# Kernel optimization log

Hardware: AMD Instinct MI355X
Metric: run time of the kernel (lower is better)

Reference implementation:

```python
import jax, jax.numpy as jnp
import numpy as np

B, S, K, N = 4, 2048, 4096, 4096


def setup_inputs() -> dict:
    key = jax.random.key(0)
    kx, kw = jax.random.split(key)
    # int8 activations and weights in [-127, 127), matching torch.randint(-127,127,...)
    x = jax.random.randint(kx, (B, S, K), -127, 127, dtype=jnp.int32).astype(jnp.int8)
    weight = jax.random.randint(kw, (N, K), -127, 127, dtype=jnp.int32).astype(jnp.int8)
    bias = jnp.zeros((1, N), dtype=jnp.int32)
    out_scale = jnp.ones((), dtype=jnp.float32)
    bias_scale = jnp.ones((), dtype=jnp.float32)
    return {"x": x, "weight": weight, "bias": bias,
            "out_scale": out_scale, "bias_scale": bias_scale}


def reference(x, weight, bias, out_scale, bias_scale):
    # Flatten leading dims: [B, S, K] -> [M, K]
    x_shape = x.shape
    x2 = x.reshape(-1, x_shape[-1])
    acc = jax.lax.dot_general(
        x2, weight,
        dimension_numbers=(((1,), (1,)), ((), ())),
        preferred_element_type=jnp.int32,
    )  # [M, N] int32
    # Fused epilogue: y = round(out_scale * acc + bias_scale * bias) -> int32
    y = jnp.round(acc.astype(jnp.float32) * out_scale
                  + bias.astype(jnp.float32) * bias_scale).astype(jnp.int32)
    return y.reshape(*x_shape[:-1], -1)
```

## Files before the change

kernel.cpp:

```cpp
#include <hip/hip_runtime.h>
#include <stdint.h>


typedef int v4i __attribute__((ext_vector_type(4)));

#define BM 128
#define BN 128
#define BK 64
#define KK 4096

__global__ __launch_bounds__(256)
void pack_i32_to_i8(const v4i* __restrict__ src, int* __restrict__ dst, int n4) {
    int i = blockIdx.x * blockDim.x + threadIdx.x;
    if (i >= n4) return;
    v4i a = src[i];
    dst[i] = (a[0] & 0xff) | ((a[1] & 0xff) << 8) | ((a[2] & 0xff) << 16) | (a[3] << 24);
}

__device__ __forceinline__ void gld_lds16(const void* g, void* lds) {
    __builtin_amdgcn_global_load_lds(
        (const __attribute__((address_space(1))) unsigned int*)g,
        (__attribute__((address_space(3))) unsigned int*)lds,
        16, 0, 0);
}

__global__ __launch_bounds__(256, 2)
void w8a8_gemm_kernel(const int8_t* __restrict__ X,
                      const int8_t* __restrict__ W,
                      const int*    __restrict__ bias,
                      const float*  __restrict__ out_scale_p,
                      const float*  __restrict__ bias_scale_p,
                      int*          __restrict__ Y,
                      int M, int N)
{
    __shared__ __align__(16) int8_t sA[BM * BK];
    __shared__ __align__(16) int8_t sB[BN * BK];

    const int t = threadIdx.x;
    const int w = t >> 6;
    const int l = t & 63;
    const int wm = w >> 1;
    const int wn = w & 1;

    const int bn = blockIdx.x * BN;
    const int bm = blockIdx.y * BM;

    const float out_scale  = *out_scale_p;
    const float bias_scale = *bias_scale_p;

    const int8_t* Abase = X + (size_t)bm * KK;
    const int8_t* Bbase = W + (size_t)bn * KK;

    const int c0 = w * 64 + l;
    const int c1 = 256 + c0;
    const int ga0 = (c0 >> 2) * KK + (c0 & 3) * 16;
    const int ga1 = (c1 >> 2) * KK + (c1 & 3) * 16;

    int8_t* sA_r0 = sA + w * 1024;
    int8_t* sA_r1 = sA + 4096 + w * 1024;
    int8_t* sB_r0 = sB + w * 1024;
    int8_t* sB_r1 = sB + 4096 + w * 1024;

    const int tm   = l & 15;
    const int quad = l >> 4;
    const int ldsA = (wm * 64 + tm) * BK + quad * 16;
    const int ldsB = (wn * 64 + tm) * BK + quad * 16;

    v4i acc[4][4];
    const v4i vzero = {0, 0, 0, 0};
#pragma unroll
    for (int i = 0; i < 4; i++)
#pragma unroll
        for (int j = 0; j < 4; j++)
            acc[i][j] = vzero;

    for (int k0 = 0; k0 < KK; k0 += BK) {
        gld_lds16(Abase + ga0 + k0, sA_r0);
        gld_lds16(Abase + ga1 + k0, sA_r1);
        gld_lds16(Bbase + ga0 + k0, sB_r0);
        gld_lds16(Bbase + ga1 + k0, sB_r1);
        __syncthreads();

        v4i a[4], b[4];
#pragma unroll
        for (int i = 0; i < 4; i++)
            a[i] = *(const v4i*)(sA + ldsA + i * 16 * BK);
#pragma unroll
        for (int j = 0; j < 4; j++)
            b[j] = *(const v4i*)(sB + ldsB + j * 16 * BK);

#pragma unroll
        for (int i = 0; i < 4; i++)
#pragma unroll
            for (int j = 0; j < 4; j++)
                acc[i][j] = __builtin_amdgcn_mfma_i32_16x16x64_i8(a[i], b[j], acc[i][j], 0, 0, 0);

        __syncthreads();
    }

#pragma unroll
    for (int j = 0; j < 4; j++) {
        const int n = bn + wn * 64 + j * 16 + tm;
        const float bb = (float)bias[n] * bias_scale;
#pragma unroll
        for (int i = 0; i < 4; i++) {
            const int mb = bm + wm * 64 + i * 16 + quad * 4;
#pragma unroll
            for (int r = 0; r < 4; r++) {
                const float v = (float)acc[i][j][r] * out_scale + bb;
                Y[(size_t)(mb + r) * N + n] = (int)rintf(v);
            }
        }
    }
}

extern "C" void kernel_launch(void* const* d_in, const int* in_sizes, int n_in,
                              void* d_out, int out_size, void* d_ws, size_t ws_size,
                              hipStream_t stream) {
    const int* x32 = (const int*)d_in[0];
    const int* w32 = (const int*)d_in[1];
    const int*    bias = (const int*)d_in[2];
    const float*  os   = (const float*)d_in[3];
    const float*  bs   = (const float*)d_in[4];
    int* out = (int*)d_out;

    const int K = KK;
    const int M = in_sizes[0] / K;
    const int N = in_sizes[1] / K;
    const int nx = in_sizes[0];
    const int nw = in_sizes[1];

    int8_t* x8 = (int8_t*)d_ws;
    int8_t* w8 = x8 + (size_t)nx;

    pack_i32_to_i8<<<dim3(nx / 4 / 256), dim3(256), 0, stream>>>((const v4i*)x32, (int*)x8, nx / 4);
    pack_i32_to_i8<<<dim3(nw / 4 / 256), dim3(256), 0, stream>>>((const v4i*)w32, (int*)w8, nw / 4);

    dim3 grid(N / BN, M / BM);
    dim3 block(256);
    hipLaunchKernelGGL(w8a8_gemm_kernel, grid, block, 0, stream,
                       x8, w8, bias, os, bs, out, M, N);
}
```

Measured before the change: 421.3 us.

## Double K tile to 128 and XOR-swizzle LDS layout to avoid bank conflicts

Raises the K tile from 64 to 128 bytes, so each global-to-LDS load round and barrier pair covers twice the MFMA work. The 16-byte chunks are stored in LDS with an XOR swizzle keyed on the row, and the fragment reads apply the same swizzle to cut LDS bank conflicts on the strided 128-byte rows. The goal is to halve sync overhead per unit of compute and improve LDS read throughput. In exchange, shared memory per block doubles to 32 KB, which may affect occupancy, and there is still no double buffering.

```diff
diff --git a/kernel.cpp b/kernel.cpp
--- a/kernel.cpp
+++ b/kernel.cpp
@@ -6,7 +6,7 @@
 
 #define BM 128
 #define BN 128
-#define BK 64
+#define BK 128
 #define KK 4096
 
 __global__ __launch_bounds__(256)
@@ -51,20 +51,20 @@
     const int8_t* Abase = X + (size_t)bm * KK;
     const int8_t* Bbase = W + (size_t)bn * KK;
 
-    const int c0 = w * 64 + l;
-    const int c1 = 256 + c0;
-    const int ga0 = (c0 >> 2) * KK + (c0 & 3) * 16;
-    const int ga1 = (c1 >> 2) * KK + (c1 & 3) * 16;
-
-    int8_t* sA_r0 = sA + w * 1024;
-    int8_t* sA_r1 = sA + 4096 + w * 1024;
-    int8_t* sB_r0 = sB + w * 1024;
-    int8_t* sB_r1 = sB + 4096 + w * 1024;
+    int ga[4];
+#pragma unroll
+    for (int r = 0; r < 4; r++) {
+        const int c   = r * 256 + w * 64 + l;
+        const int row = c >> 3;
+        const int j   = c & 7;
+        ga[r] = row * KK + ((j ^ (row & 7)) << 4);
+    }
 
     const int tm   = l & 15;
     const int quad = l >> 4;
-    const int ldsA = (wm * 64 + tm) * BK + quad * 16;
-    const int ldsB = (wn * 64 + tm) * BK + quad * 16;
+    const int s3   = tm & 7;
+    const int rowA = (wm * 64 + tm) * BK;
+    const int rowB = (wn * 64 + tm) * BK;
 
     v4i acc[4][4];
     const v4i vzero = {0, 0, 0, 0};
@@ -75,25 +75,29 @@
             acc[i][j] = vzero;
 
     for (int k0 = 0; k0 < KK; k0 += BK) {
-        gld_lds16(Abase + ga0 + k0, sA_r0);
-        gld_lds16(Abase + ga1 + k0, sA_r1);
-        gld_lds16(Bbase + ga0 + k0, sB_r0);
-        gld_lds16(Bbase + ga1 + k0, sB_r1);
+#pragma unroll
+        for (int r = 0; r < 4; r++) {
+            gld_lds16(Abase + ga[r] + k0, sA + r * 4096 + w * 1024);
+            gld_lds16(Bbase + ga[r] + k0, sB + r * 4096 + w * 1024);
+        }
         __syncthreads();
 
-        v4i a[4], b[4];
 #pragma unroll
-        for (int i = 0; i < 4; i++)
-            a[i] = *(const v4i*)(sA + ldsA + i * 16 * BK);
+        for (int h = 0; h < 2; h++) {
+            const int xo = (((h << 2) + quad) ^ s3) << 4;
+            v4i a[4], b[4];
 #pragma unroll
-        for (int j = 0; j < 4; j++)
-            b[j] = *(const v4i*)(sB + ldsB + j * 16 * BK);
-
-#pragma unroll
-        for (int i = 0; i < 4; i++)
+            for (int i = 0; i < 4; i++)
+                a[i] = *(const v4i*)(sA + rowA + i * 16 * BK + xo);
 #pragma unroll
             for (int j = 0; j < 4; j++)
-                acc[i][j] = __builtin_amdgcn_mfma_i32_16x16x64_i8(a[i], b[j], acc[i][j], 0, 0, 0);
+                b[j] = *(const v4i*)(sB + rowB + j * 16 * BK + xo);
+#pragma unroll
+            for (int i = 0; i < 4; i++)
+#pragma unroll
+                for (int j = 0; j < 4; j++)
+                    acc[i][j] = __builtin_amdgcn_mfma_i32_16x16x64_i8(a[i], b[j], acc[i][j], 0, 0, 0);
+        }
 
         __syncthreads();
     }
```

Result: faster. 387.1 us (-8.1%).
